# Performance work log

Measured on AMD Instinct MI355X. Metric: run time of the kernel, lower is better.

The kernel has to match this reference:

```python
import jax, jax.numpy as jnp
import numpy as np

B, OBS, LAT, NXT, E, HG, H = 8192, 128, 32, 128, 8, 256, 256


def setup_inputs() -> dict:
    key = jax.random.key(0)
    ks = jax.random.split(key, 20)
    d_in = OBS + LAT

    def w(k, shape, fan_in):
        return jax.random.uniform(k, shape, jnp.float32, -1.0, 1.0) * (np.sqrt(3.0) / np.sqrt(fan_in)).astype(np.float32)

    inp = {
        "x": jax.random.normal(ks[0], (B, OBS), jnp.float32),
        "z": jax.random.normal(ks[1], (B, LAT), jnp.float32),
        # gating MLP: (obs+lat) -> hg -> hg -> hg -> E
        "gw0": w(ks[2], (d_in, HG), d_in), "gb0": jnp.zeros((HG,), jnp.float32),
        "gw1": w(ks[3], (HG, HG), HG),    "gb1": jnp.zeros((HG,), jnp.float32),
        "gw2": w(ks[4], (HG, HG), HG),    "gb2": jnp.zeros((HG,), jnp.float32),
        "gw3": w(ks[5], (HG, E), HG),     "gb3": jnp.zeros((E,), jnp.float32),
        # expert weight stacks (kaiming-uniform-style init, bias = 0.01)
        "w0": w(ks[6], (E, d_in, H), d_in * H),      "b0": jnp.full((E, H), 0.01, jnp.float32),
        "w1": w(ks[7], (E, H + LAT, H), (H + LAT) * H), "b1": jnp.full((E, H), 0.01, jnp.float32),
        "w2": w(ks[8], (E, H + LAT, NXT), (H + LAT) * NXT), "b2": jnp.full((E, NXT), 0.01, jnp.float32),
    }
    return inp


def reference(x, z, gw0, gb0, gw1, gb1, gw2, gb2, gw3, gb3, w0, b0, w1, b1, w2, b2):
    xz = jnp.concatenate((x, z), axis=1)  # [B, obs+lat]
    # gating MLP (ELU activations, linear head) -> softmax coefficients over experts
    g = jax.nn.elu(xz @ gw0 + gb0)
    g = jax.nn.elu(g @ gw1 + gb1)
    g = jax.nn.elu(g @ gw2 + gb2)
    coef = jax.nn.softmax(g @ gw3 + gb3, axis=1)  # [B, E]

    layer_out = x
    for w, b, act in ((w0, b0, jax.nn.elu), (w1, b1, jax.nn.elu), (w2, b2, None)):
        inp = jnp.concatenate((layer_out, z), axis=1)  # [B, i]
        # coefficient-weighted expert mixing fused with the per-sample matvec:
        # equals (coef @ flat_weight).view(B,i,o) consumed by baddbmm in the original
        out = jnp.einsum('bi,eio,be->bo', inp, w, coef) + coef @ b
        layer_out = act(out) if act is not None else out
    return layer_out
```

## Files before the change

### kernel.cpp

```cpp
#include <hip/hip_runtime.h>
#include <hip/hip_bf16.h>

typedef _Float16 half_t;
typedef __attribute__((ext_vector_type(8))) _Float16 half8;
typedef __attribute__((ext_vector_type(4))) _Float16 half4;
typedef __attribute__((ext_vector_type(4))) float float4v;

#define BSZ 8192
#define NT 512

__device__ __forceinline__ float elu_fast(float v) {
    return v > 0.f ? v : (__expf(v) - 1.f);
}

template <int EXP, int CH, int NSTR, int ACT, int DST>
__device__ __forceinline__ void layer_pipe(
    const half_t* sSrc, int sstr, const half_t* __restrict__ W, int Npad,
    const float* __restrict__ bias, int biasN, const float* sCf,
    half_t* sDst, int dstr, float* __restrict__ gOut, int ldg,
    int row0, int wv, int l15, int quad) {
    constexpr int K = CH * 32;
    constexpr int SPW = NSTR / 8;
    constexpr int TOT = SPW * CH;
    const size_t estr = (size_t)Npad * K;

    half8 bb[3][EXP];
    half8 aa[2][2];
    float4v acc[EXP][2];

    {
        const half_t* wp = &W[(size_t)(wv * 16 + l15) * K + quad * 8];
#pragma unroll
        for (int e = 0; e < EXP; ++e) bb[0][e] = *(const half8*)&wp[e * estr];
    }
    if (TOT > 1) {
        const int p1 = 1 / CH, c1 = 1 % CH;
        const half_t* wp = &W[(size_t)((wv + p1 * 8) * 16 + l15) * K + c1 * 32 + quad * 8];
#pragma unroll
        for (int e = 0; e < EXP; ++e) bb[1][e] = *(const half8*)&wp[e * estr];
    }
    aa[0][0] = *(const half8*)&sSrc[l15 * sstr + quad * 8];
    aa[0][1] = *(const half8*)&sSrc[(16 + l15) * sstr + quad * 8];

#pragma unroll
    for (int it = 0; it < TOT; ++it) {
        const int p = it / CH, c = it - p * CH;
        if (it + 2 < TOT) {
            const int p2 = (it + 2) / CH, c2 = (it + 2) % CH;
            const half_t* wp =
                &W[(size_t)((wv + p2 * 8) * 16 + l15) * K + c2 * 32 + quad * 8];
#pragma unroll
            for (int e = 0; e < EXP; ++e)
                bb[(it + 2) % 3][e] = *(const half8*)&wp[e * estr];
        }
        if (it + 1 < TOT) {
            const int c1 = (it + 1) % CH;
            aa[(it + 1) & 1][0] = *(const half8*)&sSrc[l15 * sstr + c1 * 32 + quad * 8];
            aa[(it + 1) & 1][1] =
                *(const half8*)&sSrc[(16 + l15) * sstr + c1 * 32 + quad * 8];
        }
        if (c == 0) {
#pragma unroll
            for (int e = 0; e < EXP; ++e) {
                acc[e][0] = (float4v){0.f, 0.f, 0.f, 0.f};
                acc[e][1] = (float4v){0.f, 0.f, 0.f, 0.f};
            }
        }
#pragma unroll
        for (int e = 0; e < EXP; ++e) {
            acc[e][0] = __builtin_amdgcn_mfma_f32_16x16x32_f16(aa[it & 1][0], bb[it % 3][e],
                                                               acc[e][0], 0, 0, 0);
            acc[e][1] = __builtin_amdgcn_mfma_f32_16x16x32_f16(aa[it & 1][1], bb[it % 3][e],
                                                               acc[e][1], 0, 0, 0);
        }
        if (c == CH - 1) {
            const int col = (wv + p * 8) * 16 + l15;
            float bv[EXP];
#pragma unroll
            for (int e = 0; e < EXP; ++e) bv[e] = bias[e * biasN + col];
#pragma unroll
            for (int mt = 0; mt < 2; ++mt)
#pragma unroll
                for (int r = 0; r < 4; ++r) {
                    const int rl = mt * 16 + quad * 4 + r;
                    float val;
                    if (EXP == 1) {
                        val = acc[0][mt][r] + bv[0];
                    } else {
                        const float4v c0 = *(const float4v*)&sCf[rl * 8];
                        const float4v c1 = *(const float4v*)&sCf[rl * 8 + 4];
                        val = 0.f;
#pragma unroll
                        for (int e = 0; e < 4; ++e) val += c0[e] * (acc[e][mt][r] + bv[e]);
#pragma unroll
                        for (int e = 4; e < 8; ++e)
                            val += c1[e - 4] * (acc[e][mt][r] + bv[e]);
                    }
                    if (DST == 0) {
                        if (ACT) val = elu_fast(val);
                        sDst[rl * dstr + col] = (half_t)val;
                    } else {
                        gOut[(size_t)(row0 + rl) * ldg + col] = val;
                    }
                }
        }
    }
}

template <int CH>
__device__ __forceinline__ void layer_logits(
    const half_t* sSrc, int sstr, const half_t* __restrict__ W,
    const float* __restrict__ bias, float* sLog, int wv, int l15, int quad) {
    if (wv != 0) return;
    constexpr int K = CH * 32;
    float4v acc[2] = {(float4v){0.f, 0.f, 0.f, 0.f}, (float4v){0.f, 0.f, 0.f, 0.f}};
    const half_t* wb = &W[(size_t)l15 * K + quad * 8];
#pragma unroll
    for (int c = 0; c < CH; ++c) {
        half8 a0 = *(const half8*)&sSrc[l15 * sstr + c * 32 + quad * 8];
        half8 a1 = *(const half8*)&sSrc[(16 + l15) * sstr + c * 32 + quad * 8];
        half8 b = *(const half8*)&wb[c * 32];
        acc[0] = __builtin_amdgcn_mfma_f32_16x16x32_f16(a0, b, acc[0], 0, 0, 0);
        acc[1] = __builtin_amdgcn_mfma_f32_16x16x32_f16(a1, b, acc[1], 0, 0, 0);
    }
    if (l15 < 8) {
        const float bv = bias[l15];
#pragma unroll
        for (int mt = 0; mt < 2; ++mt)
#pragma unroll
            for (int r = 0; r < 4; ++r) {
                const int rl = mt * 16 + quad * 4 + r;
                sLog[rl * 8 + l15] = acc[mt][r] + bv;
            }
    }
}

__global__ __launch_bounds__(NT) void fused_mann(
    const float* __restrict__ x, const float* __restrict__ z,
    const half_t* __restrict__ Wg0, const half_t* __restrict__ Wg1,
    const half_t* __restrict__ Wg2, const half_t* __restrict__ Wg3,
    const float* __restrict__ gb0, const float* __restrict__ gb1,
    const float* __restrict__ gb2, const float* __restrict__ gb3,
    const half_t* __restrict__ W0, const half_t* __restrict__ W1,
    const half_t* __restrict__ W2, const float* __restrict__ b0,
    const float* __restrict__ b1, const float* __restrict__ b2,
    float* __restrict__ out) {
    __shared__ __align__(16) half_t sA0[32 * 168];
    __shared__ __align__(16) half_t sBuf0[32 * 296];
    __shared__ __align__(16) half_t sBuf1[32 * 296];
    __shared__ float sLog[32 * 8];
    __shared__ float sCf[32 * 8];

    const int tid = threadIdx.x;
    const int row0 = blockIdx.x * 32;
    const int lane = tid & 63, wv = tid >> 6;
    const int l15 = lane & 15, quad = lane >> 4;

    for (int i = tid; i < 32 * 160; i += NT) {
        int r = i / 160, c = i % 160;
        float v = (c < 128) ? x[(size_t)(row0 + r) * 128 + c]
                            : z[(size_t)(row0 + r) * 32 + (c - 128)];
        sA0[r * 168 + c] = (half_t)v;
    }
    for (int i = tid; i < 32 * 32; i += NT) {
        int r = i >> 5, c = i & 31;
        half_t h = (half_t)z[(size_t)(row0 + r) * 32 + c];
        sBuf0[r * 296 + 256 + c] = h;
        sBuf1[r * 296 + 256 + c] = h;
    }
    __syncthreads();

    layer_pipe<1, 5, 16, 1, 0>(sA0, 168, Wg0, 256, gb0, 256, nullptr, sBuf0, 296,
                               nullptr, 0, row0, wv, l15, quad);
    __syncthreads();
    layer_pipe<1, 8, 16, 1, 0>(sBuf0, 296, Wg1, 256, gb1, 256, nullptr, sBuf1, 296,
                               nullptr, 0, row0, wv, l15, quad);
    __syncthreads();
    layer_pipe<1, 8, 16, 1, 0>(sBuf1, 296, Wg2, 256, gb2, 256, nullptr, sBuf0, 296,
                               nullptr, 0, row0, wv, l15, quad);
    __syncthreads();
    layer_logits<8>(sBuf0, 296, Wg3, gb3, sLog, wv, l15, quad);
    __syncthreads();
    if (tid < 32) {
        float v[8], m = -1e30f;
#pragma unroll
        for (int e = 0; e < 8; ++e) { v[e] = sLog[tid * 8 + e]; m = fmaxf(m, v[e]); }
        float sum = 0.f;
#pragma unroll
        for (int e = 0; e < 8; ++e) { v[e] = __expf(v[e] - m); sum += v[e]; }
        float inv = 1.f / sum;
#pragma unroll
        for (int e = 0; e < 8; ++e) sCf[tid * 8 + e] = v[e] * inv;
    }
    __syncthreads();
    layer_pipe<8, 5, 16, 1, 0>(sA0, 168, W0, 256, b0, 256, sCf, sBuf1, 296,
                               nullptr, 0, row0, wv, l15, quad);
    __syncthreads();
    layer_pipe<8, 9, 16, 1, 0>(sBuf1, 296, W1, 256, b1, 256, sCf, sBuf0, 296,
                               nullptr, 0, row0, wv, l15, quad);
    __syncthreads();
    layer_pipe<8, 9, 8, 0, 2>(sBuf0, 296, W2, 128, b2, 128, sCf, nullptr, 0,
                              out, 128, row0, wv, l15, quad);
}

struct WDesc { const float* src; half_t* dst; int K, N, Npad, blk0; };
struct WPack { WDesc d[7]; };

__global__ __launch_bounds__(256) void conv_w_all(WPack pk) {
    __shared__ float t[32][33];
    const int bid = blockIdx.x;
    int di = 0;
#pragma unroll
    for (int i = 1; i < 7; ++i)
        if (bid >= pk.d[i].blk0) di = i;
    const WDesc d = pk.d[di];
    const int ntiles = d.Npad / 32, ktiles = d.K / 32;
    int local = bid - d.blk0;
    const int e = local / (ktiles * ntiles);
    local %= ktiles * ntiles;
    const int k0 = (local / ntiles) * 32, n0 = (local % ntiles) * 32;
    const int tr = threadIdx.x >> 3;
    const int tc = (threadIdx.x & 7) * 4;

    float4 v = {0.f, 0.f, 0.f, 0.f};
    if (n0 + tc < d.N)
        v = *(const float4*)&d.src[((size_t)e * d.K + k0 + tr) * d.N + n0 + tc];
    t[tr][tc] = v.x; t[tr][tc + 1] = v.y; t[tr][tc + 2] = v.z; t[tr][tc + 3] = v.w;
    __syncthreads();
    half4 h;
#pragma unroll
    for (int i = 0; i < 4; ++i) h[i] = (half_t)t[tc + i][tr];
    *(half4*)&d.dst[((size_t)e * d.Npad + n0 + tr) * d.K + k0 + tc] = h;
}

extern "C" void kernel_launch(void* const* d_in, const int* in_sizes, int n_in,
                              void* d_out, int out_size, void* d_ws, size_t ws_size,
                              hipStream_t stream) {
    const float* x   = (const float*)d_in[0];
    const float* z   = (const float*)d_in[1];
    const float* gw0 = (const float*)d_in[2];
    const float* gb0 = (const float*)d_in[3];
    const float* gw1 = (const float*)d_in[4];
    const float* gb1 = (const float*)d_in[5];
    const float* gw2 = (const float*)d_in[6];
    const float* gb2 = (const float*)d_in[7];
    const float* gw3 = (const float*)d_in[8];
    const float* gb3 = (const float*)d_in[9];
    const float* w0  = (const float*)d_in[10];
    const float* b0  = (const float*)d_in[11];
    const float* w1  = (const float*)d_in[12];
    const float* b1  = (const float*)d_in[13];
    const float* w2  = (const float*)d_in[14];
    const float* b2  = (const float*)d_in[15];

    char* p = (char*)d_ws;
    auto take = [&](size_t bytes) { char* r = p; p += bytes; return r; };
    half_t* Wg0 = (half_t*)take((size_t)256 * 160 * 2);
    half_t* Wg1 = (half_t*)take((size_t)256 * 256 * 2);
    half_t* Wg2 = (half_t*)take((size_t)256 * 256 * 2);
    half_t* Wg3 = (half_t*)take((size_t)32 * 256 * 2);
    half_t* W0  = (half_t*)take((size_t)8 * 256 * 160 * 2);
    half_t* W1  = (half_t*)take((size_t)8 * 256 * 288 * 2);
    half_t* W2  = (half_t*)take((size_t)8 * 128 * 288 * 2);
    float* out  = (float*)d_out;

    WPack pk;
    int blk = 0;
    auto mk = [&](int i, const float* s, half_t* dst, int K, int N, int Npad, int E) {
        pk.d[i] = WDesc{s, dst, K, N, Npad, blk};
        blk += E * (K / 32) * (Npad / 32);
    };
    mk(0, gw0, Wg0, 160, 256, 256, 1);
    mk(1, gw1, Wg1, 256, 256, 256, 1);
    mk(2, gw2, Wg2, 256, 256, 256, 1);
    mk(3, gw3, Wg3, 256, 8, 32, 1);
    mk(4, w0, W0, 160, 256, 256, 8);
    mk(5, w1, W1, 288, 256, 256, 8);
    mk(6, w2, W2, 288, 128, 128, 8);

    conv_w_all<<<dim3(blk), dim3(256), 0, stream>>>(pk);
    fused_mann<<<dim3(BSZ / 32), dim3(NT), 0, stream>>>(
        x, z, Wg0, Wg1, Wg2, Wg3, gb0, gb1, gb2, gb3,
        W0, W1, W2, b0, b1, b2, out);
}
```

Before: 158.5 us.

## Double block threads to 16 waves, one column strip each, experts split into halves

Block size goes from 512 to 1024 threads, so each wave now owns a single 16-column strip instead of looping over two strips. Expert layers now process the 8 experts in two passes of 4, carrying a partial weighted sum in registers between passes. This cuts per-wave register pressure and raises the number of waves available to hide latency. The risks are idle waves on the narrower final layer and the logits stage, fewer blocks per CU at 1024 threads, and __launch_bounds__ possibly needing an update to match.

```diff
diff --git a/kernel.cpp b/kernel.cpp
--- a/kernel.cpp
+++ b/kernel.cpp
@@ -7,100 +7,99 @@
 typedef __attribute__((ext_vector_type(4))) float float4v;
 
 #define BSZ 8192
-#define NT 512
+#define NT 1024
 
 __device__ __forceinline__ float elu_fast(float v) {
     return v > 0.f ? v : (__expf(v) - 1.f);
 }
 
-template <int EXP, int CH, int NSTR, int ACT, int DST>
-__device__ __forceinline__ void layer_pipe(
+template <int EXPP, int NPASS, int CH, int NSTR, int ACT, int DST>
+__device__ __forceinline__ void layer_run(
     const half_t* sSrc, int sstr, const half_t* __restrict__ W, int Npad,
     const float* __restrict__ bias, int biasN, const float* sCf,
     half_t* sDst, int dstr, float* __restrict__ gOut, int ldg,
     int row0, int wv, int l15, int quad) {
+    if (wv >= NSTR) return;
     constexpr int K = CH * 32;
-    constexpr int SPW = NSTR / 8;
-    constexpr int TOT = SPW * CH;
+    constexpr int TOT = NPASS * CH;
     const size_t estr = (size_t)Npad * K;
-
-    half8 bb[3][EXP];
+    const half_t* wbase = &W[(size_t)(wv * 16 + l15) * K + quad * 8];
+
+    half8 bb[3][EXPP];
     half8 aa[2][2];
-    float4v acc[EXP][2];
-
+    float4v acc[EXPP][2];
+    float part[2][4];
+
+#pragma unroll
+    for (int e = 0; e < EXPP; ++e) bb[0][e] = *(const half8*)&wbase[(size_t)e * estr];
     {
-        const half_t* wp = &W[(size_t)(wv * 16 + l15) * K + quad * 8];
-#pragma unroll
-        for (int e = 0; e < EXP; ++e) bb[0][e] = *(const half8*)&wp[e * estr];
-    }
-    if (TOT > 1) {
-        const int p1 = 1 / CH, c1 = 1 % CH;
-        const half_t* wp = &W[(size_t)((wv + p1 * 8) * 16 + l15) * K + c1 * 32 + quad * 8];
-#pragma unroll
-        for (int e = 0; e < EXP; ++e) bb[1][e] = *(const half8*)&wp[e * estr];
+        const half_t* wp = wbase + 32;
+#pragma unroll
+        for (int e = 0; e < EXPP; ++e) bb[1][e] = *(const half8*)&wp[(size_t)e * estr];
     }
     aa[0][0] = *(const half8*)&sSrc[l15 * sstr + quad * 8];
     aa[0][1] = *(const half8*)&sSrc[(16 + l15) * sstr + quad * 8];
 
 #pragma unroll
     for (int it = 0; it < TOT; ++it) {
-        const int p = it / CH, c = it - p * CH;
+        const int h = it / CH, c = it - h * CH;
         if (it + 2 < TOT) {
-            const int p2 = (it + 2) / CH, c2 = (it + 2) % CH;
-            const half_t* wp =
-                &W[(size_t)((wv + p2 * 8) * 16 + l15) * K + c2 * 32 + quad * 8];
-#pragma unroll
-            for (int e = 0; e < EXP; ++e)
-                bb[(it + 2) % 3][e] = *(const half8*)&wp[e * estr];
+            const int h2 = (it + 2) / CH, c2 = (it + 2) % CH;
+            const half_t* wp = wbase + (size_t)(h2 * EXPP) * estr + c2 * 32;
+#pragma unroll
+            for (int e = 0; e < EXPP; ++e)
+                bb[(it + 2) % 3][e] = *(const half8*)&wp[(size_t)e * estr];
         }
         if (it + 1 < TOT) {
-            const int c1 = (it + 1) % CH;
-            aa[(it + 1) & 1][0] = *(const half8*)&sSrc[l15 * sstr + c1 * 32 + quad * 8];
+            const int c1n = (it + 1) % CH;
+            aa[(it + 1) & 1][0] = *(const half8*)&sSrc[l15 * sstr + c1n * 32 + quad * 8];
             aa[(it + 1) & 1][1] =
-                *(const half8*)&sSrc[(16 + l15) * sstr + c1 * 32 + quad * 8];
+                *(const half8*)&sSrc[(16 + l15) * sstr + c1n * 32 + quad * 8];
         }
         if (c == 0) {
 #pragma unroll
-            for (int e = 0; e < EXP; ++e) {
+            for (int e = 0; e < EXPP; ++e) {
                 acc[e][0] = (float4v){0.f, 0.f, 0.f, 0.f};
                 acc[e][1] = (float4v){0.f, 0.f, 0.f, 0.f};
             }
         }
 #pragma unroll
-        for (int e = 0; e < EXP; ++e) {
+        for (int e = 0; e < EXPP; ++e) {
             acc[e][0] = __builtin_amdgcn_mfma_f32_16x16x32_f16(aa[it & 1][0], bb[it % 3][e],
                                                                acc[e][0], 0, 0, 0);
             acc[e][1] = __builtin_amdgcn_mfma_f32_16x16x32_f16(aa[it & 1][1], bb[it % 3][e],
                                                                acc[e][1], 0, 0, 0);
         }
         if (c == CH - 1) {
-            const int col = (wv + p * 8) * 16 + l15;
-            float bv[EXP];
-#pragma unroll
-            for (int e = 0; e < EXP; ++e) bv[e] = bias[e * biasN + col];
+            const int col = wv * 16 + l15;
+            const int eoff = h * EXPP;
+            float bv[EXPP];
+#pragma unroll
+            for (int e = 0; e < EXPP; ++e) bv[e] = bias[(eoff + e) * biasN + col];
 #pragma unroll
             for (int mt = 0; mt < 2; ++mt)
 #pragma unroll
                 for (int r = 0; r < 4; ++r) {
                     const int rl = mt * 16 + quad * 4 + r;
                     float val;
-                    if (EXP == 1) {
+                    if (EXPP == 1) {
                         val = acc[0][mt][r] + bv[0];
                     } else {
-                        const float4v c0 = *(const float4v*)&sCf[rl * 8];
-                        const float4v c1 = *(const float4v*)&sCf[rl * 8 + 4];
                         val = 0.f;
 #pragma unroll
-                        for (int e = 0; e < 4; ++e) val += c0[e] * (acc[e][mt][r] + bv[e]);
-#pragma unroll
-                        for (int e = 4; e < 8; ++e)
-                            val += c1[e - 4] * (acc[e][mt][r] + bv[e]);
+                        for (int e = 0; e < EXPP; ++e)
+                            val += sCf[rl * 8 + eoff + e] * (acc[e][mt][r] + bv[e]);
                     }
-                    if (DST == 0) {
-                        if (ACT) val = elu_fast(val);
-                        sDst[rl * dstr + col] = (half_t)val;
+                    if (NPASS == 2 && h == 0) {
+                        part[mt][r] = val;
                     } else {
-                        gOut[(size_t)(row0 + rl) * ldg + col] = val;
+                        if (NPASS == 2) val += part[mt][r];
+                        if (DST == 0) {
+                            if (ACT) val = elu_fast(val);
+                            sDst[rl * dstr + col] = (half_t)val;
+                        } else {
+                            gOut[(size_t)(row0 + rl) * ldg + col] = val;
+                        }
                     }
                 }
         }
@@ -170,14 +169,14 @@
     }
     __syncthreads();
 
-    layer_pipe<1, 5, 16, 1, 0>(sA0, 168, Wg0, 256, gb0, 256, nullptr, sBuf0, 296,
-                               nullptr, 0, row0, wv, l15, quad);
-    __syncthreads();
-    layer_pipe<1, 8, 16, 1, 0>(sBuf0, 296, Wg1, 256, gb1, 256, nullptr, sBuf1, 296,
-                               nullptr, 0, row0, wv, l15, quad);
-    __syncthreads();
-    layer_pipe<1, 8, 16, 1, 0>(sBuf1, 296, Wg2, 256, gb2, 256, nullptr, sBuf0, 296,
-                               nullptr, 0, row0, wv, l15, quad);
+    layer_run<1, 1, 5, 16, 1, 0>(sA0, 168, Wg0, 256, gb0, 256, nullptr, sBuf0, 296,
+                                 nullptr, 0, row0, wv, l15, quad);
+    __syncthreads();
+    layer_run<1, 1, 8, 16, 1, 0>(sBuf0, 296, Wg1, 256, gb1, 256, nullptr, sBuf1, 296,
+                                 nullptr, 0, row0, wv, l15, quad);
+    __syncthreads();
+    layer_run<1, 1, 8, 16, 1, 0>(sBuf1, 296, Wg2, 256, gb2, 256, nullptr, sBuf0, 296,
+                                 nullptr, 0, row0, wv, l15, quad);
     __syncthreads();
     layer_logits<8>(sBuf0, 296, Wg3, gb3, sLog, wv, l15, quad);
     __syncthreads();
@@ -193,14 +192,14 @@
         for (int e = 0; e < 8; ++e) sCf[tid * 8 + e] = v[e] * inv;
     }
     __syncthreads();
-    layer_pipe<8, 5, 16, 1, 0>(sA0, 168, W0, 256, b0, 256, sCf, sBuf1, 296,
-                               nullptr, 0, row0, wv, l15, quad);
-    __syncthreads();
-    layer_pipe<8, 9, 16, 1, 0>(sBuf1, 296, W1, 256, b1, 256, sCf, sBuf0, 296,
-                               nullptr, 0, row0, wv, l15, quad);
-    __syncthreads();
-    layer_pipe<8, 9, 8, 0, 2>(sBuf0, 296, W2, 128, b2, 128, sCf, nullptr, 0,
-                              out, 128, row0, wv, l15, quad);
+    layer_run<4, 2, 5, 16, 1, 0>(sA0, 168, W0, 256, b0, 256, sCf, sBuf1, 296,
+                                 nullptr, 0, row0, wv, l15, quad);
+    __syncthreads();
+    layer_run<4, 2, 9, 16, 1, 0>(sBuf1, 296, W1, 256, b1, 256, sCf, sBuf0, 296,
+                                 nullptr, 0, row0, wv, l15, quad);
+    __syncthreads();
+    layer_run<4, 2, 9, 8, 0, 2>(sBuf0, 296, W2, 128, b2, 128, sCf, nullptr, 0,
+                                out, 128, row0, wv, l15, quad);
 }
 
 struct WDesc { const float* src; half_t* dst; int K, N, Npad, blk0; };
```

After: 170.4 us. +7.5%, slower.
